# Kernel optimization log

Measured on AMD Instinct MI355X. Metric: run time of the kernel, lower is better.

The kernel has to match this reference:

```python
import jax, jax.numpy as jnp
import numpy as np

INF = 1e9  # large finite sentinel (avoid inf arithmetic in potentials)


def _hungarian(cost):
    """Exact linear sum assignment (Jonker-Volgenant style shortest augmenting
    path, O(N^3)) on a single [N, N] cost matrix. Returns col_ind (int32 [N])
    such that row i is matched to column col_ind[i] with minimal total cost
    (same solution as scipy.optimize.linear_sum_assignment up to ties).
    Column index n is a virtual 'start' column (e-maxx formulation)."""
    n = cost.shape[0]

    def row_body(i, carry):
        u, v, p = carry  # u: row potentials [n]; v: col potentials [n+1]; p[j]: row assigned to col j (-1 free)
        p = p.at[n].set(i)
        state = (u, v, p,
                 jnp.full(n + 1, INF, cost.dtype),   # minv
                 jnp.zeros(n + 1, dtype=bool),       # used
                 jnp.zeros(n + 1, dtype=jnp.int32),  # way (parent col on path)
                 jnp.int32(n))                       # j0 current col

        def cond(st):
            _, _, p_, _, _, _, j0 = st
            return p_[j0] >= 0  # stop when we reach a free column

        def body(st):
            u_, v_, p_, minv, used, way, j0 = st
            used = used.at[j0].set(True)
            i0 = p_[j0]
            cur = cost[i0] - u_[i0] - v_[:n]          # reduced costs of row i0 [n]
            cur = jnp.where(used[:n], INF, cur)
            better = cur < minv[:n]
            minv = minv.at[:n].set(jnp.where(better, cur, minv[:n]))
            way = way.at[:n].set(jnp.where(better, j0, way[:n]))
            masked = jnp.where(used[:n], INF, minv[:n])
            j1 = jnp.argmin(masked).astype(jnp.int32)
            delta = masked[j1]
            # dual update: used cols raise row potential, others shrink minv
            u_ = u_.at[p_].add(jnp.where(used, delta, jnp.zeros((), cost.dtype)))
            v_ = jnp.where(used, v_ - delta, v_)
            minv = jnp.where(used, minv, minv - delta)
            return (u_, v_, p_, minv, used, way, j1)

        u, v, p, _, _, way, j0 = jax.lax.while_loop(cond, body, state)

        # augment along the alternating path back to the virtual column
        def cond2(s):
            j, _ = s
            return j != n

        def body2(s):
            j, p_ = s
            j_prev = way[j]
            return j_prev, p_.at[j].set(p_[j_prev])

        _, p = jax.lax.while_loop(cond2, body2, (j0, p))
        return (u, v, p)

    u0 = jnp.zeros(n, cost.dtype)
    v0 = jnp.zeros(n + 1, cost.dtype)
    p0 = jnp.full(n + 1, -1, dtype=jnp.int32)
    _, _, p = jax.lax.fori_loop(0, n, row_body, (u0, v0, p0))
    # p[j] = row matched to col j  ->  col_ind[row] = j
    col_ind = jnp.zeros(n, jnp.int32).at[p[:n]].set(jnp.arange(n, dtype=jnp.int32))
    return col_ind


def setup_inputs() -> dict:
    key = jax.random.key(0)
    k1, k2 = jax.random.split(key)
    B, N, D = 2048, 24, 256
    slots = jax.random.normal(k1, (B, N, D), dtype=jnp.float32)
    prev_slots = jax.random.normal(k2, (B, N, D), dtype=jnp.float32)
    return {"slots": slots, "prev_slots": prev_slots}


def reference(slots, prev_slots):
    """HungarianPredictor.forward with similarity='cosine': reorder current
    slots to align with prev_slots ordering via optimal 1-1 matching."""
    eps = 1e-12  # torch F.normalize eps
    pn = prev_slots / jnp.maximum(
        jnp.linalg.norm(prev_slots, axis=-1, keepdims=True), eps)
    cn = slots / jnp.maximum(
        jnp.linalg.norm(slots, axis=-1, keepdims=True), eps)
    # cost[b, i, j] = 1 - <prev_i, curr_j>   [B, N, N]
    cost = 1.0 - jnp.einsum('bnd,bmd->bnm', pn, cn)
    col = jax.vmap(_hungarian)(jax.lax.stop_gradient(cost))  # [B, N] int32
    reordered = jax.vmap(lambda s, c: s[c])(slots, col)       # gather per batch
    return reordered
```

## Files before the change

kernel.cpp:

```cpp
#include <hip/hip_runtime.h>
#include <math.h>

#define N    24
#define D    256
#define BLK  256
#define NB   4
#define CTS  28
#define INFV 1e9f

__device__ __forceinline__ int readlane_i(int x, int l) {
    return __builtin_amdgcn_readlane(x, l);
}
__device__ __forceinline__ float readlane_f(float x, int l) {
    return __uint_as_float((unsigned)__builtin_amdgcn_readlane((int)__float_as_uint(x), l));
}

__device__ __forceinline__ unsigned wave_min32(unsigned x) {
    unsigned t;
    t = (unsigned)__builtin_amdgcn_update_dpp((int)x, (int)x, 0xB1,  0xF, 0xF, false); x = t < x ? t : x;
    t = (unsigned)__builtin_amdgcn_update_dpp((int)x, (int)x, 0x4E,  0xF, 0xF, false); x = t < x ? t : x;
    t = (unsigned)__builtin_amdgcn_update_dpp((int)x, (int)x, 0x114, 0xF, 0xF, false); x = t < x ? t : x;
    t = (unsigned)__builtin_amdgcn_update_dpp((int)x, (int)x, 0x118, 0xF, 0xF, false); x = t < x ? t : x;
    t = (unsigned)__builtin_amdgcn_update_dpp((int)x, (int)x, 0x142, 0xF, 0xF, false); x = t < x ? t : x;
    return x;
}

#define DOT4(a, b) ((a).x*(b).x + (a).y*(b).y + (a).z*(b).z + (a).w*(b).w)
#define LGKM0() __asm__ volatile("s_waitcnt lgkmcnt(0)" ::: "memory")

__global__ __launch_bounds__(BLK) void hungarian_fused(
    const float* __restrict__ slots,
    const float* __restrict__ prev,
    float* __restrict__ out, int B)
{
    __shared__ __align__(16) float costT[NB][N][CTS];
    __shared__ int winner[NB][N];
    __shared__ int colw[NB][N];

    const int tid  = threadIdx.x;
    const int lane = tid & 63;
    const int wv   = tid >> 6;
    const int bw   = blockIdx.x * NB + wv;
    if (bw >= B) return;

    const int rg = lane >> 3;
    const int cg = lane & 7;
    const float4* pA = (const float4*)(prev  + (size_t)bw * N * D) + rg * 3 * (D / 4);
    const float4* pC = (const float4*)(slots + (size_t)bw * N * D) + cg * 3 * (D / 4);

    float s00=0,s01=0,s02=0,s10=0,s11=0,s12=0,s20=0,s21=0,s22=0;
    float pa0=0,pa1=0,pa2=0,pc0=0,pc1=0,pc2=0;
    #pragma unroll 2
    for (int k = 0; k < 64; ++k) {
        float4 a0 = pA[k], a1 = pA[64+k], a2 = pA[128+k];
        float4 b0 = pC[k], b1 = pC[64+k], b2 = pC[128+k];
        s00 += DOT4(a0,b0); s01 += DOT4(a0,b1); s02 += DOT4(a0,b2);
        s10 += DOT4(a1,b0); s11 += DOT4(a1,b1); s12 += DOT4(a1,b2);
        s20 += DOT4(a2,b0); s21 += DOT4(a2,b1); s22 += DOT4(a2,b2);
        pa0 += DOT4(a0,a0); pa1 += DOT4(a1,a1); pa2 += DOT4(a2,a2);
        pc0 += DOT4(b0,b0); pc1 += DOT4(b1,b1); pc2 += DOT4(b2,b2);
    }
    float ira0 = 1.0f / fmaxf(sqrtf(pa0), 1e-12f);
    float ira1 = 1.0f / fmaxf(sqrtf(pa1), 1e-12f);
    float ira2 = 1.0f / fmaxf(sqrtf(pa2), 1e-12f);
    float irc0 = 1.0f / fmaxf(sqrtf(pc0), 1e-12f);
    float irc1 = 1.0f / fmaxf(sqrtf(pc1), 1e-12f);
    float irc2 = 1.0f / fmaxf(sqrtf(pc2), 1e-12f);

    {
        float* ct = &costT[wv][0][0];
        const int cb = cg * 3, rb = rg * 3;
        ct[(cb+0)*CTS + rb+0] = 1.0f - s00*ira0*irc0;
        ct[(cb+1)*CTS + rb+0] = 1.0f - s01*ira0*irc1;
        ct[(cb+2)*CTS + rb+0] = 1.0f - s02*ira0*irc2;
        ct[(cb+0)*CTS + rb+1] = 1.0f - s10*ira1*irc0;
        ct[(cb+1)*CTS + rb+1] = 1.0f - s11*ira1*irc1;
        ct[(cb+2)*CTS + rb+1] = 1.0f - s12*ira1*irc2;
        ct[(cb+0)*CTS + rb+2] = 1.0f - s20*ira2*irc0;
        ct[(cb+1)*CTS + rb+2] = 1.0f - s21*ira2*irc1;
        ct[(cb+2)*CTS + rb+2] = 1.0f - s22*ira2*irc2;
    }
    LGKM0();

    const bool isCol = (lane < N);
    const int  jj    = isCol ? lane : 0;
    float cq[24];
    {
        const float4* cp4 = (const float4*)&costT[wv][jj][0];
        #pragma unroll
        for (int r = 0; r < 6; ++r) {
            float4 q = cp4[r];
            cq[r*4+0] = q.x; cq[r*4+1] = q.y; cq[r*4+2] = q.z; cq[r*4+3] = q.w;
        }
    }

    float cm = cq[0]; int ri = 0;
    #pragma unroll
    for (int i = 1; i < N; ++i) { if (cq[i] < cm) { cm = cq[i]; ri = i; } }

    if (isCol) winner[wv][lane] = -1;
    LGKM0();
    if (isCol) winner[wv][ri] = lane;
    LGKM0();
    int p = -1;
    if (isCol && winner[wv][ri] == lane) p = ri;
    const int widx = isCol ? lane : 0;
    unsigned long long mm = __ballot(isCol && winner[wv][widx] >= 0);
    unsigned freeRows = (~(unsigned)mm) & ((1u << N) - 1);

    float uu  = 0.0f;
    float v   = isCol ? cm : INFV;
    int   way = -1;

    while (freeRows) {
        const int f = (int)__builtin_ctz(freeRows);
        freeRows &= freeRows - 1;

        float minv  = INFV;
        bool  used  = false;
        bool  inTree = false;
        int   s_j0 = -1;
        int   s_i0 = f;
        float s_u0 = readlane_f(uu, f);
        int   j1   = 0;

        while (true) {
            inTree = inTree || (lane == s_i0);
            used   = used   || (lane == s_j0);

            float cij;
            switch (s_i0) {
                case 0:  cij = cq[0];  break;  case 1:  cij = cq[1];  break;
                case 2:  cij = cq[2];  break;  case 3:  cij = cq[3];  break;
                case 4:  cij = cq[4];  break;  case 5:  cij = cq[5];  break;
                case 6:  cij = cq[6];  break;  case 7:  cij = cq[7];  break;
                case 8:  cij = cq[8];  break;  case 9:  cij = cq[9];  break;
                case 10: cij = cq[10]; break;  case 11: cij = cq[11]; break;
                case 12: cij = cq[12]; break;  case 13: cij = cq[13]; break;
                case 14: cij = cq[14]; break;  case 15: cij = cq[15]; break;
                case 16: cij = cq[16]; break;  case 17: cij = cq[17]; break;
                case 18: cij = cq[18]; break;  case 19: cij = cq[19]; break;
                case 20: cij = cq[20]; break;  case 21: cij = cq[21]; break;
                case 22: cij = cq[22]; break;  default: cij = cq[23]; break;
            }
            float cur = cij - s_u0 - v;
            bool  act = isCol && !used;
            if (act && cur < minv) { minv = cur; way = s_j0; }
            float masked = act ? minv : INFV;

            unsigned key = __float_as_uint(masked);
            key ^= (unsigned)((int)key >> 31) | 0x80000000u;
            key  = (key & 0xFFFFFFC0u) | (unsigned)lane;
            unsigned kmin = (unsigned)readlane_i((int)wave_min32(key), 31);
            j1 = (int)(kmin & 63u);

            float delta = readlane_f(masked, j1);
            int   i0n   = readlane_i(p, j1);
            float u0n   = readlane_f(uu, i0n & 31);

            if (inTree) uu += delta;
            if (used) v -= delta;
            else if (act) minv -= delta;

            if (i0n < 0) break;
            s_j0 = j1; s_i0 = i0n; s_u0 = u0n;
        }

        int jcur = j1;
        while (true) {
            int wj   = readlane_i(way, jcur);
            int pnew = (wj < 0) ? f : readlane_i(p, wj);
            if (lane == jcur) p = pnew;
            if (wj < 0) break;
            jcur = wj;
        }
    }

    if (isCol) colw[wv][p] = lane;
    LGKM0();

    const float4* sg4 = (const float4*)(slots + (size_t)bw * N * D);
    float4*       og4 = (float4*)(out + (size_t)bw * N * D);
    #pragma unroll
    for (int i = 0; i < N; ++i) {
        int c = colw[wv][i];
        og4[i * 64 + lane] = sg4[c * 64 + lane];
    }
}

extern "C" void kernel_launch(void* const* d_in, const int* in_sizes, int n_in,
                              void* d_out, int out_size, void* d_ws, size_t ws_size,
                              hipStream_t stream) {
    const float* slots = (const float*)d_in[0];
    const float* prev  = (const float*)d_in[1];
    float* out = (float*)d_out;
    int B = in_sizes[0] / (N * D);
    int grid = (B + NB - 1) / NB;
    hungarian_fused<<<grid, BLK, 0, stream>>>(slots, prev, out, B);
}
```

Before: 193.9 us.

## Add auction-style augmenting row reduction before shortest-path Hungarian phase

Inserts a Jonker-Volgenant augmenting row reduction pass. Each free row finds its best and second-best reduced-cost columns through a two-minimum wave reduction, takes the best column, and displaces that column's previous owner. The pass is capped at 64 steps, and rows that tie or hit the cap fall back to the existing shortest augmenting path loop. This is meant to cut the number of expensive Dijkstra-style augmentations. The risks are extra serial reduction steps and subtle dual-feasibility issues that could change assignments when ties occur.

```diff
diff --git a/kernel.cpp b/kernel.cpp
--- a/kernel.cpp
+++ b/kernel.cpp
@@ -23,6 +23,47 @@
     t = (unsigned)__builtin_amdgcn_update_dpp((int)x, (int)x, 0x118, 0xF, 0xF, false); x = t < x ? t : x;
     t = (unsigned)__builtin_amdgcn_update_dpp((int)x, (int)x, 0x142, 0xF, 0xF, false); x = t < x ? t : x;
     return x;
+}
+
+__device__ __forceinline__ void wave_min2_32(unsigned x, unsigned& r1, unsigned& r2) {
+    unsigned m1 = x, m2 = 0xFFFFFFFFu;
+    unsigned t1, t2, lo, hi;
+#define MIN2_STEP(pat)                                                          \
+    t1 = (unsigned)__builtin_amdgcn_update_dpp((int)m1, (int)m1, pat, 0xF, 0xF, false); \
+    t2 = (unsigned)__builtin_amdgcn_update_dpp((int)m2, (int)m2, pat, 0xF, 0xF, false); \
+    lo = t1 < m1 ? t1 : m1; hi = t1 < m1 ? m1 : t1;                              \
+    m2 = m2 < t2 ? m2 : t2; m2 = m2 < hi ? m2 : hi;                              \
+    m1 = lo;
+    MIN2_STEP(0xB1)
+    MIN2_STEP(0x4E)
+    MIN2_STEP(0x114)
+    MIN2_STEP(0x118)
+    MIN2_STEP(0x142)
+#undef MIN2_STEP
+    r1 = m1; r2 = m2;
+}
+
+__device__ __forceinline__ float csel(const float* cq, int i0) {
+    switch (i0) {
+        case 0:  return cq[0];   case 1:  return cq[1];
+        case 2:  return cq[2];   case 3:  return cq[3];
+        case 4:  return cq[4];   case 5:  return cq[5];
+        case 6:  return cq[6];   case 7:  return cq[7];
+        case 8:  return cq[8];   case 9:  return cq[9];
+        case 10: return cq[10];  case 11: return cq[11];
+        case 12: return cq[12];  case 13: return cq[13];
+        case 14: return cq[14];  case 15: return cq[15];
+        case 16: return cq[16];  case 17: return cq[17];
+        case 18: return cq[18];  case 19: return cq[19];
+        case 20: return cq[20];  case 21: return cq[21];
+        case 22: return cq[22];  default: return cq[23];
+    }
+}
+
+__device__ __forceinline__ unsigned packkey(float x, int lane) {
+    unsigned key = __float_as_uint(x);
+    key ^= (unsigned)((int)key >> 31) | 0x80000000u;
+    return (key & 0xFFFFFFC0u) | (unsigned)lane;
 }
 
 #define DOT4(a, b) ((a).x*(b).x + (a).y*(b).y + (a).z*(b).z + (a).w*(b).w)
@@ -112,6 +153,35 @@
     float v   = isCol ? cm : INFV;
     int   way = -1;
 
+    {
+        unsigned arFree  = freeRows;
+        unsigned leftover = 0;
+        int steps = 0;
+        while (arFree) {
+            int i = (int)__builtin_ctz(arFree);
+            arFree &= arFree - 1;
+            while (true) {
+                if (++steps > 64) { leftover |= 1u << i; break; }
+                float cij = csel(cq, i);
+                float w   = isCol ? (cij - v) : INFV;
+                unsigned k1, k2;
+                wave_min2_32(packkey(w, lane), k1, k2);
+                k1 = (unsigned)readlane_i((int)k1, 31);
+                k2 = (unsigned)readlane_i((int)k2, 31);
+                int   j1 = (int)(k1 & 63u), j2 = (int)(k2 & 63u);
+                float u1 = readlane_f(w, j1);
+                float u2 = readlane_f(w, j2);
+                if (!(u1 < u2)) { leftover |= 1u << i; break; }
+                int i1 = readlane_i(p, j1);
+                if (lane == j1) { v -= (u2 - u1); p = i; }
+                if (lane == i)  uu = u2;
+                if (i1 < 0) break;
+                i = i1;
+            }
+        }
+        freeRows = leftover | arFree;
+    }
+
     while (freeRows) {
         const int f = (int)__builtin_ctz(freeRows);
         freeRows &= freeRows - 1;
@@ -128,30 +198,14 @@
             inTree = inTree || (lane == s_i0);
             used   = used   || (lane == s_j0);
 
-            float cij;
-            switch (s_i0) {
-                case 0:  cij = cq[0];  break;  case 1:  cij = cq[1];  break;
-                case 2:  cij = cq[2];  break;  case 3:  cij = cq[3];  break;
-                case 4:  cij = cq[4];  break;  case 5:  cij = cq[5];  break;
-                case 6:  cij = cq[6];  break;  case 7:  cij = cq[7];  break;
-                case 8:  cij = cq[8];  break;  case 9:  cij = cq[9];  break;
-                case 10: cij = cq[10]; break;  case 11: cij = cq[11]; break;
-                case 12: cij = cq[12]; break;  case 13: cij = cq[13]; break;
-                case 14: cij = cq[14]; break;  case 15: cij = cq[15]; break;
-                case 16: cij = cq[16]; break;  case 17: cij = cq[17]; break;
-                case 18: cij = cq[18]; break;  case 19: cij = cq[19]; break;
-                case 20: cij = cq[20]; break;  case 21: cij = cq[21]; break;
-                case 22: cij = cq[22]; break;  default: cij = cq[23]; break;
-            }
+            float cij = csel(cq, s_i0);
             float cur = cij - s_u0 - v;
             bool  act = isCol && !used;
             if (act && cur < minv) { minv = cur; way = s_j0; }
             float masked = act ? minv : INFV;
 
-            unsigned key = __float_as_uint(masked);
-            key ^= (unsigned)((int)key >> 31) | 0x80000000u;
-            key  = (key & 0xFFFFFFC0u) | (unsigned)lane;
-            unsigned kmin = (unsigned)readlane_i((int)wave_min32(key), 31);
+            unsigned kmin = (unsigned)readlane_i(
+                (int)wave_min32(packkey(masked, lane)), 31);
             j1 = (int)(kmin & 63u);
 
             float delta = readlane_f(masked, j1);
```

Result: slower. 202.2 us (+4.3%).
